# Performance work log

Hardware: AMD Instinct MI355X
Metric: run time of the kernel (lower is better)

Reference implementation:

```python
import jax, jax.numpy as jnp
import numpy as np


def setup_inputs() -> dict:
    key = jax.random.key(0)
    b, l, d_model, n_head, topk = 2, 2048, 1024, 16, 32
    dh = d_model // n_head
    k0, k1, k2, k3, k4 = jax.random.split(key, 5)
    s = 1.0 / np.sqrt(d_model)
    return {
        "q_in": jax.random.normal(k0, (b, l, d_model), jnp.float32),
        "kv_in": jax.random.normal(k1, (b, l, d_model), jnp.float32),
        "w_q": jax.random.normal(k2, (d_model, d_model), jnp.float32) * s,
        "w_kv": jax.random.normal(k3, (d_model, 2 * dh), jnp.float32) * s,
        "w_concat": jax.random.normal(k4, (d_model, d_model), jnp.float32) * s,
        "topk": topk,
        "n_head": n_head,
    }


def _l2norm_seq(x):
    # F.normalize default dim=1 -> normalize along the sequence axis (faithful to source)
    n = jnp.sqrt(jnp.sum(x * x, axis=1, keepdims=True))
    return x / jnp.maximum(n, 1e-12)


def reference(q_in, kv_in, w_q, w_kv, w_concat, topk, n_head):
    b, l, d_model = q_in.shape
    dh = d_model // n_head
    scale = 1.0 / np.sqrt(dh)

    q = q_in @ w_q                                  # (b, l, d_model)
    kv = kv_in @ w_kv                               # (b, l, 2*dh)
    k, v = kv[..., :dh], kv[..., dh:]
    k, v = _l2norm_seq(k), _l2norm_seq(v)           # (b, l, dh) single shared KV head

    q = q.reshape(b, l, n_head, dh).transpose(0, 2, 1, 3)  # (b, h, l, dh)

    # one similarity matrix reused for local attention and kNN retrieval
    sims = jnp.einsum('bhld,bmd->bhlm', q, k)       # (b, h, l, m)

    # local SDPA (KV head broadcast over query heads)
    local = jnp.einsum('bhlm,bmd->bhld', jax.nn.softmax(sims * scale, axis=-1), v)

    # exact inner-product kNN over stored keys (faiss memory stores k only,
    # so retrieved key == retrieved value == nearest stored key vectors)
    _, idx = jax.lax.top_k(sims, topk)              # (b, h, l, topk)
    mem = jax.vmap(lambda kk, ii: kk[ii])(k, idx)   # (b, h, l, topk, dh)

    s_ret = jnp.einsum('bhld,bhltd->bhlt', q, mem) * scale
    retrieved = jnp.einsum('bhlt,bhltd->bhld', jax.nn.softmax(s_ret, axis=-1), mem)

    out = (local + retrieved).transpose(0, 2, 1, 3).reshape(b, l, d_model)
    return out @ w_concat
```

## Files before the change

kernel.cpp:

```cpp
#include <hip/hip_runtime.h>
#include <cstddef>
#include <cstring>

#define B_    2
#define L_    2048
#define DM_   1024
#define NH_   16
#define DH_   64
#define SCALE_ 0.125f

typedef __bf16 bf16x8 __attribute__((ext_vector_type(8)));
typedef float  f32x4  __attribute__((ext_vector_type(4)));
typedef unsigned short ushort8v __attribute__((ext_vector_type(8)));
typedef unsigned short ushort4v __attribute__((ext_vector_type(4)));
typedef unsigned long long u64;
typedef unsigned int u32;

__device__ __forceinline__ u32 flipf(float f) {
    u32 u = __float_as_uint(f);
    return (u & 0x80000000u) ? ~u : (u | 0x80000000u);
}
__device__ __forceinline__ float bf2f(unsigned short u) {
    return __uint_as_float(((u32)u) << 16);
}
__device__ __forceinline__ unsigned short f2bf(float f) {
    __bf16 h = (__bf16)f;
    unsigned short u;
    __builtin_memcpy(&u, &h, 2);
    return u;
}
__device__ __forceinline__ u32 flip16(unsigned short u) {
    return (u & 0x8000u) ? (u32)(~u & 0xffffu) : (u32)(u | 0x8000u);
}
__device__ __forceinline__ unsigned short unflip16(u32 k) {
    return (k & 0x8000u) ? (unsigned short)(k ^ 0x8000u) : (unsigned short)(~k & 0xffffu);
}

__global__ __launch_bounds__(256)
void wsplit3(const float* __restrict__ W, unsigned short* __restrict__ w1,
             unsigned short* __restrict__ w2, unsigned short* __restrict__ w3,
             int K, int N) {
    const int n0 = blockIdx.x << 6;
    const int k0 = blockIdx.y << 6;
    const int t  = threadIdx.x;
    __shared__ float s[64][65];
    const int rr = t >> 4;
    const int c4 = (t & 15) << 2;
    #pragma unroll
    for (int rep = 0; rep < 4; ++rep) {
        int k = rr + (rep << 4);
        float4 x = *(const float4*)(W + (size_t)(k0 + k) * N + n0 + c4);
        s[k][c4+0] = x.x; s[k][c4+1] = x.y; s[k][c4+2] = x.z; s[k][c4+3] = x.w;
    }
    __syncthreads();
    #pragma unroll
    for (int rep = 0; rep < 4; ++rep) {
        int n = rr + (rep << 4);
        ushort4v h, m, l;
        #pragma unroll
        for (int j = 0; j < 4; ++j) {
            float x = s[c4 + j][n];
            unsigned short hh = f2bf(x);
            float r = x - bf2f(hh);
            unsigned short mm = f2bf(r);
            float r2 = r - bf2f(mm);
            h[j] = hh; m[j] = mm; l[j] = f2bf(r2);
        }
        size_t o = (size_t)(n0 + n) * K + k0 + c4;
        *(ushort4v*)(w1 + o) = h;
        *(ushort4v*)(w2 + o) = m;
        *(ushort4v*)(w3 + o) = l;
    }
}

__global__ __launch_bounds__(256)
void gemm6p(const float* __restrict__ A, const unsigned short* __restrict__ w1,
            const unsigned short* __restrict__ w2, const unsigned short* __restrict__ w3,
            float* __restrict__ C, int N, int K) {
    __shared__ __align__(16) unsigned short sA[3][128][40];
    __shared__ __align__(16) unsigned short sW[3][64][40];
    const int t    = threadIdx.x;
    const int wv   = t >> 6;
    const int lane = t & 63;
    const int quad = lane >> 4;
    const int n15  = lane & 15;
    const int bm = blockIdx.y << 7;
    const int bn = blockIdx.x << 6;
    const int wm = (wv >> 1) << 6;
    const int wn = (wv & 1) << 5;
    f32x4 acc[4][2];
    #pragma unroll
    for (int i = 0; i < 4; ++i)
        #pragma unroll
        for (int j = 0; j < 2; ++j)
            #pragma unroll
            for (int r = 0; r < 4; ++r) acc[i][j][r] = 0.f;

    const int ar  = t >> 1,  acg = (t & 1) << 4;
    const int wr  = t >> 2,  wcg = (t & 3) << 3;
    const float* Ap = A + (size_t)(bm + ar) * K + acg;
    const size_t wo = (size_t)(bn + wr) * K + wcg;

    for (int k0 = 0; k0 < K; k0 += 32) {
        float4 a0 = *(const float4*)(Ap + k0);
        float4 a1 = *(const float4*)(Ap + k0 + 4);
        float4 a2 = *(const float4*)(Ap + k0 + 8);
        float4 a3 = *(const float4*)(Ap + k0 + 12);
        ushort8v u1 = *(const ushort8v*)(w1 + wo + k0);
        ushort8v u2 = *(const ushort8v*)(w2 + wo + k0);
        ushort8v u3 = *(const ushort8v*)(w3 + wo + k0);
        __syncthreads();
        {
            float av[16] = {a0.x,a0.y,a0.z,a0.w, a1.x,a1.y,a1.z,a1.w,
                            a2.x,a2.y,a2.z,a2.w, a3.x,a3.y,a3.z,a3.w};
            ushort8v h0, h1, m0, m1, lo0, lo1;
            #pragma unroll
            for (int i = 0; i < 8; ++i) {
                float x = av[i];
                unsigned short hh = f2bf(x);
                float r = x - bf2f(hh);
                unsigned short mm = f2bf(r);
                h0[i] = hh; m0[i] = mm; lo0[i] = f2bf(r - bf2f(mm));
                float y = av[8 + i];
                unsigned short hh2 = f2bf(y);
                float r2 = y - bf2f(hh2);
                unsigned short mm2 = f2bf(r2);
                h1[i] = hh2; m1[i] = mm2; lo1[i] = f2bf(r2 - bf2f(mm2));
            }
            *(ushort8v*)&sA[0][ar][acg]     = h0;
            *(ushort8v*)&sA[0][ar][acg + 8] = h1;
            *(ushort8v*)&sA[1][ar][acg]     = m0;
            *(ushort8v*)&sA[1][ar][acg + 8] = m1;
            *(ushort8v*)&sA[2][ar][acg]     = lo0;
            *(ushort8v*)&sA[2][ar][acg + 8] = lo1;
            *(ushort8v*)&sW[0][wr][wcg] = u1;
            *(ushort8v*)&sW[1][wr][wcg] = u2;
            *(ushort8v*)&sW[2][wr][wcg] = u3;
        }
        __syncthreads();
        bf16x8 af[3][4];
        #pragma unroll
        for (int mi = 0; mi < 4; ++mi) {
            af[0][mi] = *(const bf16x8*)&sA[0][wm + (mi << 4) + n15][quad << 3];
            af[1][mi] = *(const bf16x8*)&sA[1][wm + (mi << 4) + n15][quad << 3];
            af[2][mi] = *(const bf16x8*)&sA[2][wm + (mi << 4) + n15][quad << 3];
        }
        #pragma unroll
        for (int nj = 0; nj < 2; ++nj) {
            bf16x8 wf1 = *(const bf16x8*)&sW[0][wn + (nj << 4) + n15][quad << 3];
            bf16x8 wf2 = *(const bf16x8*)&sW[1][wn + (nj << 4) + n15][quad << 3];
            bf16x8 wf3 = *(const bf16x8*)&sW[2][wn + (nj << 4) + n15][quad << 3];
            #pragma unroll
            for (int mi = 0; mi < 4; ++mi) {
                acc[mi][nj] = __builtin_amdgcn_mfma_f32_16x16x32_bf16(af[0][mi], wf1, acc[mi][nj], 0, 0, 0);
                acc[mi][nj] = __builtin_amdgcn_mfma_f32_16x16x32_bf16(af[0][mi], wf2, acc[mi][nj], 0, 0, 0);
                acc[mi][nj] = __builtin_amdgcn_mfma_f32_16x16x32_bf16(af[1][mi], wf1, acc[mi][nj], 0, 0, 0);
                acc[mi][nj] = __builtin_amdgcn_mfma_f32_16x16x32_bf16(af[1][mi], wf2, acc[mi][nj], 0, 0, 0);
                acc[mi][nj] = __builtin_amdgcn_mfma_f32_16x16x32_bf16(af[0][mi], wf3, acc[mi][nj], 0, 0, 0);
                acc[mi][nj] = __builtin_amdgcn_mfma_f32_16x16x32_bf16(af[2][mi], wf1, acc[mi][nj], 0, 0, 0);
            }
        }
    }
    #pragma unroll
    for (int mi = 0; mi < 4; ++mi)
        #pragma unroll
        for (int nj = 0; nj < 2; ++nj)
            #pragma unroll
            for (int r = 0; r < 4; ++r)
                C[(size_t)(bm + wm + (mi << 4) + (quad << 2) + r) * N
                  + bn + wn + (nj << 4) + n15] = acc[mi][nj][r];
}

__global__ __launch_bounds__(256)
void gemm3p(const float* __restrict__ A, const unsigned short* __restrict__ w1,
            const unsigned short* __restrict__ w2,
            float* __restrict__ C, int N, int K) {
    __shared__ __align__(16) unsigned short sA[2][128][40];
    __shared__ __align__(16) unsigned short sW[2][64][40];
    const int t    = threadIdx.x;
    const int wv   = t >> 6;
    const int lane = t & 63;
    const int quad = lane >> 4;
    const int n15  = lane & 15;
    const int bm = blockIdx.y << 7;
    const int bn = blockIdx.x << 6;
    const int wm = (wv >> 1) << 6;
    const int wn = (wv & 1) << 5;
    f32x4 acc[4][2];
    #pragma unroll
    for (int i = 0; i < 4; ++i)
        #pragma unroll
        for (int j = 0; j < 2; ++j)
            #pragma unroll
            for (int r = 0; r < 4; ++r) acc[i][j][r] = 0.f;

    const int ar  = t >> 1,  acg = (t & 1) << 4;
    const int wr  = t >> 2,  wcg = (t & 3) << 3;
    const float* Ap = A + (size_t)(bm + ar) * K + acg;
    const size_t wo = (size_t)(bn + wr) * K + wcg;

    for (int k0 = 0; k0 < K; k0 += 32) {
        float4 a0 = *(const float4*)(Ap + k0);
        float4 a1 = *(const float4*)(Ap + k0 + 4);
        float4 a2 = *(const float4*)(Ap + k0 + 8);
        float4 a3 = *(const float4*)(Ap + k0 + 12);
        ushort8v u1 = *(const ushort8v*)(w1 + wo + k0);
        ushort8v u2 = *(const ushort8v*)(w2 + wo + k0);
        __syncthreads();
        {
            float av[16] = {a0.x,a0.y,a0.z,a0.w, a1.x,a1.y,a1.z,a1.w,
                            a2.x,a2.y,a2.z,a2.w, a3.x,a3.y,a3.z,a3.w};
            ushort8v h0, h1, l0v, l1v;
            #pragma unroll
            for (int i = 0; i < 8; ++i) {
                float x = av[i];
                unsigned short hh = f2bf(x);
                h0[i] = hh; l0v[i] = f2bf(x - bf2f(hh));
                float y = av[8 + i];
                unsigned short hh2 = f2bf(y);
                h1[i] = hh2; l1v[i] = f2bf(y - bf2f(hh2));
            }
            *(ushort8v*)&sA[0][ar][acg]     = h0;
            *(ushort8v*)&sA[0][ar][acg + 8] = h1;
            *(ushort8v*)&sA[1][ar][acg]     = l0v;
            *(ushort8v*)&sA[1][ar][acg + 8] = l1v;
            *(ushort8v*)&sW[0][wr][wcg] = u1;
            *(ushort8v*)&sW[1][wr][wcg] = u2;
        }
        __syncthreads();
        bf16x8 af[2][4];
        #pragma unroll
        for (int mi = 0; mi < 4; ++mi) {
            af[0][mi] = *(const bf16x8*)&sA[0][wm + (mi << 4) + n15][quad << 3];
            af[1][mi] = *(const bf16x8*)&sA[1][wm + (mi << 4) + n15][quad << 3];
        }
        #pragma unroll
        for (int nj = 0; nj < 2; ++nj) {
            bf16x8 wf1 = *(const bf16x8*)&sW[0][wn + (nj << 4) + n15][quad << 3];
            bf16x8 wf2 = *(const bf16x8*)&sW[1][wn + (nj << 4) + n15][quad << 3];
            #pragma unroll
            for (int mi = 0; mi < 4; ++mi) {
                acc[mi][nj] = __builtin_amdgcn_mfma_f32_16x16x32_bf16(af[0][mi], wf1, acc[mi][nj], 0, 0, 0);
                acc[mi][nj] = __builtin_amdgcn_mfma_f32_16x16x32_bf16(af[0][mi], wf2, acc[mi][nj], 0, 0, 0);
                acc[mi][nj] = __builtin_amdgcn_mfma_f32_16x16x32_bf16(af[1][mi], wf1, acc[mi][nj], 0, 0, 0);
            }
        }
    }
    #pragma unroll
    for (int mi = 0; mi < 4; ++mi)
        #pragma unroll
        for (int nj = 0; nj < 2; ++nj)
            #pragma unroll
            for (int r = 0; r < 4; ++r)
                C[(size_t)(bm + wm + (mi << 4) + (quad << 2) + r) * N
                  + bn + wn + (nj << 4) + n15] = acc[mi][nj][r];
}

__global__ __launch_bounds__(256)
void col_norms(const float* __restrict__ kv, float* __restrict__ invn) {
    const int bc = blockIdx.x;
    const int b  = bc >> 7;
    const int c  = bc & 127;
    const int t  = threadIdx.x;
    const float* base = kv + (size_t)b * L_ * 128 + c;
    float ss = 0.f;
    for (int l = t; l < L_; l += 256) {
        float x = base[(size_t)l * 128];
        ss += x * x;
    }
    #pragma unroll
    for (int off = 32; off; off >>= 1) ss += __shfl_xor(ss, off);
    __shared__ float red[4];
    if ((t & 63) == 0) red[t >> 6] = ss;
    __syncthreads();
    if (t == 0) {
        float tot = red[0] + red[1] + red[2] + red[3];
        invn[bc] = 1.f / fmaxf(sqrtf(tot), 1e-12f);
    }
}

__global__ __launch_bounds__(256)
void scale_kv(const float* __restrict__ kv, const float* __restrict__ invn,
              float* __restrict__ kn, __bf16* __restrict__ kh,
              __bf16* __restrict__ vT) {
    const int b  = blockIdx.y;
    const int l0 = blockIdx.x << 6;
    const int t  = threadIdx.x;
    __shared__ float s_inv[128];
    __shared__ float s_vt[64][65];
    if (t < 128) s_inv[t] = invn[b * 128 + t];
    __syncthreads();
    #pragma unroll
    for (int rep = 0; rep < 8; ++rep) {
        int idx = (rep << 8) + t;
        int li  = idx >> 5;
        int c4  = (idx & 31) << 2;
        float4 x = *(const float4*)(kv + ((size_t)(b * L_ + l0 + li)) * 128 + c4);
        x.x *= s_inv[c4]; x.y *= s_inv[c4+1]; x.z *= s_inv[c4+2]; x.w *= s_inv[c4+3];
        if (c4 < 64) {
            size_t o = ((size_t)(b * L_ + l0 + li)) * DH_ + c4;
            *(float4*)(kn + o) = x;
            kh[o+0] = (__bf16)x.x; kh[o+1] = (__bf16)x.y;
            kh[o+2] = (__bf16)x.z; kh[o+3] = (__bf16)x.w;
        } else {
            int d = c4 - 64;
            s_vt[d+0][li] = x.x; s_vt[d+1][li] = x.y; s_vt[d+2][li] = x.z; s_vt[d+3][li] = x.w;
        }
    }
    __syncthreads();
    #pragma unroll
    for (int rep = 0; rep < 4; ++rep) {
        int idx = (rep << 8) + t;
        int d   = idx >> 4;
        int j   = (idx & 15) << 2;
        size_t o = ((size_t)b * DH_ + d) * L_ + l0 + j;
        vT[o+0] = (__bf16)s_vt[d][j+0];
        vT[o+1] = (__bf16)s_vt[d][j+1];
        vT[o+2] = (__bf16)s_vt[d][j+2];
        vT[o+3] = (__bf16)s_vt[d][j+3];
    }
}

#define SST2_ 1032

__global__ __launch_bounds__(256, 4)
void attn_part(const float* __restrict__ q,
               const __bf16* __restrict__ kh,
               const __bf16* __restrict__ vT,
               float* __restrict__ attn,
               u32* __restrict__ cand,
               int* __restrict__ candC) {
    const int tile = blockIdx.x;
    const int h    = blockIdx.y;
    const int b    = blockIdx.z;
    const int l0   = tile << 4;
    const int t    = threadIdx.x;
    const int w    = t >> 6;
    const int lane = t & 63;
    const int quad = lane >> 4;
    const int n15  = lane & 15;

    __shared__ unsigned short s_sims[16 * SST2_];
    __shared__ float s_local[16][66];
    __shared__ float s_denom[16];

    {
        float* sl = &s_local[0][0];
        for (int i = t; i < 16 * 66; i += 256) sl[i] = 0.f;
        if (t < 16) s_denom[t] = 0.f;
    }

    bf16x8 qf[2];
    {
        const float* qp = q + ((size_t)(b * L_ + l0 + n15)) * DM_ + h * DH_ + (quad << 3);
        #pragma unroll
        for (int ks = 0; ks < 2; ++ks) {
            float4 x0 = *(const float4*)(qp + (ks << 5));
            float4 x1 = *(const float4*)(qp + (ks << 5) + 4);
            float xv[8] = {x0.x, x0.y, x0.z, x0.w, x1.x, x1.y, x1.z, x1.w};
            #pragma unroll
            for (int i2 = 0; i2 < 8; ++i2) qf[ks][i2] = (__bf16)xv[i2];
        }
    }

    f32x4 accL[4] = {{0,0,0,0},{0,0,0,0},{0,0,0,0},{0,0,0,0}};
    float psum = 0.f;
    float bvmax[4] = {-3e38f, -3e38f, -3e38f, -3e38f};
    int   c0[4]    = {0, 0, 0, 0};
    const __bf16* khb = kh + (size_t)b * L_ * DH_;
    const __bf16* vtb = vT + (size_t)b * DH_ * L_;
    const int rg0 = ((b * NH_ + h) * L_) + l0;

    #pragma unroll 1
    for (int hf = 0; hf < 2; ++hf) {
        #pragma unroll
        for (int g = 0; g < 4; ++g) {
            bf16x8 kf[8];
            const __bf16* kp = khb + (size_t)((hf << 10) + (w << 8) + (g << 6) + n15) * DH_ + (quad << 3);
            #pragma unroll
            for (int jj = 0; jj < 4; ++jj) {
                kf[2*jj]   = *(const bf16x8*)(kp + (size_t)(jj << 4) * DH_);
                kf[2*jj+1] = *(const bf16x8*)(kp + (size_t)(jj << 4) * DH_ + 32);
            }
            #pragma unroll
            for (int jj = 0; jj < 4; ++jj) {
                int m0 = (w << 8) + (g << 6) + (jj << 4);
                f32x4 acc = {0.f, 0.f, 0.f, 0.f};
                acc = __builtin_amdgcn_mfma_f32_16x16x32_bf16(kf[2*jj],   qf[0], acc, 0, 0, 0);
                acc = __builtin_amdgcn_mfma_f32_16x16x32_bf16(kf[2*jj+1], qf[1], acc, 0, 0, 0);
                u32 lo = (u32)f2bf(acc[0]) | ((u32)f2bf(acc[1]) << 16);
                u32 hi = (u32)f2bf(acc[2]) | ((u32)f2bf(acc[3]) << 16);
                u64 pk = ((u64)hi << 32) | lo;
                *(u64*)(s_sims + (size_t)n15 * SST2_ + m0 + (quad << 2)) = pk;
            }
        }
        __syncthreads();

        #pragma unroll 1
        for (int rr2 = 0; rr2 < 4; ++rr2) {
            const int r = (w << 2) + rr2;
            const unsigned short* srow = s_sims + r * SST2_;
            ushort8v rv[2];
            rv[0] = *(const ushort8v*)(srow + (lane << 3));
            rv[1] = *(const ushort8v*)(srow + 512 + (lane << 3));
            float bv = -3e38f;
            #pragma unroll
            for (int j = 0; j < 2; ++j)
                #pragma unroll
                for (int e = 0; e < 8; ++e) bv = fmaxf(bv, bf2f(rv[j][e]));
            bvmax[rr2] = fmaxf(bvmax[rr2], bv);
            u32* cr = cand + (size_t)(rg0 + r) * 96;
            if (hf == 0) {
                u32 key = flip16(f2bf(bv));
                u32 thr = 0;
                #pragma unroll
                for (int bp = 15; bp >= 0; --bp) {
                    u32 tt = thr | (1u << bp);
                    if (__popcll(__ballot(key >= tt)) >= 32) thr = tt;
                }
                float thrv = bf2f(unflip16(thr)) - 0.01f;
                int base = 0;
                #pragma unroll
                for (int j = 0; j < 2; ++j) {
                    #pragma unroll
                    for (int e = 0; e < 8; ++e) {
                        bool pred = bf2f(rv[j][e]) >= thrv;
                        u64 mk = __ballot(pred);
                        if (pred) {
                            int pos = base + __popcll(mk & ((1ull << lane) - 1));
                            if (pos < 96)
                                cr[pos] = ((u32)rv[j][e] << 16)
                                        | (u32)((j << 9) + (lane << 3) + e);
                        }
                        base += __popcll(mk);
                    }
                }
                c0[rr2] = base < 96 ? base : 96;
            } else {
                u32 key = flip16(f2bf(bvmax[rr2]));
                u32 thr = 0;
                #pragma unroll
                for (int bp = 15; bp >= 0; --bp) {
                    u32 tt = thr | (1u << bp);
                    if (__popcll(__ballot(key >= tt)) >= 32) thr = tt;
                }
                float thrv = bf2f(unflip16(thr)) - 0.01f;
                const int cc0 = c0[rr2];
                u32 e0 = (lane < cc0) ? cr[lane] : 0u;
                u32 e1 = (64 + lane < cc0) ? cr[64 + lane] : 0u;
                int base = 0;
                {
                    bool pred = (lane < cc0)
                              && (bf2f((unsigned short)(e0 >> 16)) >= thrv);
                    u64 mk = __ballot(pred);
                    if (pred) {
                        int pos = __popcll(mk & ((1ull << lane) - 1));
                        cr[pos] = e0;
                    }
                    base = __popcll(mk);
                }
                if (cc0 > 64) {
                    bool pred = (64 + lane < cc0)
                              && (bf2f((unsigned short)(e1 >> 16)) >= thrv);
                    u64 mk = __ballot(pred);
                    if (pred) {
                        int pos = base + __popcll(mk & ((1ull << lane) - 1));
                        if (pos < 96) cr[pos] = e1;
                    }
                    base += __popcll(mk);
                }
                #pragma unroll
                for (int j = 0; j < 2; ++j) {
                    #pragma unroll
                    for (int e = 0; e < 8; ++e) {
                        bool pred = bf2f(rv[j][e]) >= thrv;
                        u64 mk = __ballot(pred);
                        if (pred) {
                            int pos = base + __popcll(mk & ((1ull << lane) - 1));
                            if (pos < 96)
                                cr[pos] = ((u32)rv[j][e] << 16)
                                        | (u32)(1024 + (j << 9) + (lane << 3) + e);
                        }
                        base += __popcll(mk);
                    }
                }
                if (lane == 0) candC[rg0 + r] = base < 96 ? base : 96;
            }
        }

        #pragma unroll
        for (int g = 0; g < 4; ++g) {
            bf16x8 bvv[2][4];
            #pragma unroll
            for (int t2 = 0; t2 < 2; ++t2)
                #pragma unroll
                for (int nn = 0; nn < 4; ++nn)
                    bvv[t2][nn] = *(const bf16x8*)(vtb + (size_t)((nn << 4) + n15) * L_
                                  + (hf << 10) + (w << 8) + (g << 6) + (t2 << 5) + (quad << 3));
            #pragma unroll
            for (int t2 = 0; t2 < 2; ++t2) {
                int mb = (w << 8) + (g << 6) + (t2 << 5);
                ushort8v pu = *(const ushort8v*)(s_sims + n15 * SST2_ + mb + (quad << 3));
                bf16x8 af;
                #pragma unroll
                for (int e = 0; e < 8; ++e) {
                    float p = __expf(SCALE_ * bf2f(pu[e]));
                    psum += p;
                    af[e] = (__bf16)p;
                }
                #pragma unroll
                for (int nn = 0; nn < 4; ++nn)
                    accL[nn] = __builtin_amdgcn_mfma_f32_16x16x32_bf16(af, bvv[t2][nn], accL[nn], 0, 0, 0);
            }
        }
        __syncthreads();
    }

    psum += __shfl_xor(psum, 16);
    psum += __shfl_xor(psum, 32);
    if (lane < 16) atomicAdd(&s_denom[lane], psum);
    #pragma unroll
    for (int nn = 0; nn < 4; ++nn)
        #pragma unroll
        for (int rr = 0; rr < 4; ++rr)
            atomicAdd(&s_local[(quad << 2) + rr][(nn << 4) + n15], accL[nn][rr]);
    __syncthreads();

    {
        int r  = t >> 4;
        int d0 = (t & 15) << 2;
        float inv = 1.f / s_denom[r];
        float* op = attn + ((size_t)(b * L_ + l0 + r)) * DM_ + h * DH_ + d0;
        op[0] = s_local[r][d0+0] * inv;
        op[1] = s_local[r][d0+1] * inv;
        op[2] = s_local[r][d0+2] * inv;
        op[3] = s_local[r][d0+3] * inv;
    }
}

__global__ __launch_bounds__(256)
void topk_merge(const float* __restrict__ q, const float* __restrict__ kn,
                const u32* __restrict__ cand, const int* __restrict__ candC,
                float* __restrict__ attn) {
    const int wv   = threadIdx.x >> 6;
    const int lane = threadIdx.x & 63;
    const int row  = (blockIdx.x << 2) + wv;
    const int l = row & (L_ - 1);
    const int h = (row >> 11) & (NH_ - 1);
    const int b = row >> 15;
    __shared__ float s_dot[4][96];
    __shared__ __align__(16) u64 s_sel[4][32];

    const int C = candC[row];
    const u32* cr = cand + (size_t)row * 96;
    const float* knb = kn + (size_t)b * L_ * DH_;
    const float* qr  = q + ((size_t)(b * L_ + l)) * DM_ + h * DH_;

    int mreg0 = (lane < C) ? (int)(cr[lane] & 0xffffu) : 0;
    int mreg1 = (64 + lane < C) ? (int)(cr[64 + lane] & 0xffffu) : 0;

    const int cg = lane >> 4;
    const int dg = lane & 15;
    float4 qx = *(const float4*)(qr + (dg << 2));

    #pragma unroll 2
    for (int base = 0; base < C; base += 4) {
        int ci = base + cg;
        int src = ci & 63;
        int mA = __shfl(mreg0, src);
        int mB = __shfl(mreg1, src);
        int m  = (ci < 64) ? mA : mB;
        float4 kx = *(const float4*)(knb + (size_t)m * DH_ + (dg << 2));
        float p = kx.x * qx.x + kx.y * qx.y + kx.z * qx.z + kx.w * qx.w;
        p += __shfl_xor(p, 1);
        p += __shfl_xor(p, 2);
        p += __shfl_xor(p, 4);
        p += __shfl_xor(p, 8);
        if (dg == 0 && ci < C) s_dot[wv][ci] = p;
    }

    float dotA = (lane < C) ? s_dot[wv][lane] : 0.f;
    float dotB = (64 + lane < C) ? s_dot[wv][64 + lane] : 0.f;
    u32 keyA = (lane < C) ? flipf(dotA) : 0u;
    u32 keyB = (64 + lane < C) ? flipf(dotB) : 0u;

    u32 thr2 = 0;
    if (C <= 64) {
        #pragma unroll
        for (int bp = 31; bp >= 0; --bp) {
            u32 tt = thr2 | (1u << bp);
            if (__popcll(__ballot(keyA >= tt)) >= 32) thr2 = tt;
        }
    } else {
        #pragma unroll
        for (int bp = 31; bp >= 0; --bp) {
            u32 tt = thr2 | (1u << bp);
            int c2 = __popcll(__ballot(keyA >= tt)) + __popcll(__ballot(keyB >= tt));
            if (c2 >= 32) thr2 = tt;
        }
    }
    {
        bool pA = keyA >= thr2;
        u64 mkA = __ballot(pA);
        if (pA) {
            int pos = __popcll(mkA & ((1ull << lane) - 1));
            if (pos < 32) {
                float pt = __expf(SCALE_ * dotA);
                s_sel[wv][pos] = ((u64)__float_as_uint(pt) << 32) | (u32)mreg0;
            }
        }
        if (C > 64) {
            int cA = __popcll(mkA);
            bool pB = keyB >= thr2;
            u64 mkB = __ballot(pB);
            if (pB) {
                int pos = cA + __popcll(mkB & ((1ull << lane) - 1));
                if (pos < 32) {
                    float pt = __expf(SCALE_ * dotB);
                    s_sel[wv][pos] = ((u64)__float_as_uint(pt) << 32) | (u32)mreg1;
                }
            }
        }
    }
    {
        float pts[32];
        int   ms[32];
        #pragma unroll
        for (int i = 0; i < 32; ++i) {
            u64 s0 = s_sel[wv][i];
            pts[i] = __uint_as_float((u32)(s0 >> 32));
            ms[i]  = (int)(u32)(s0 & 0xffffffffu);
        }
        const float* knb2 = knb + lane;
        float kvv[32];
        #pragma unroll
        for (int i = 0; i < 32; ++i) kvv[i] = knb2[(size_t)ms[i] * DH_];
        float rs = 0.f, ret = 0.f;
        #pragma unroll
        for (int i = 0; i < 16; ++i) {
            rs  += pts[2*i] + pts[2*i+1];
            ret += pts[2*i] * kvv[2*i] + pts[2*i+1] * kvv[2*i+1];
        }
        size_t oa = ((size_t)(b * L_ + l)) * DM_ + h * DH_ + lane;
        attn[oa] = attn[oa] + ret / rs;
    }
}

extern "C" void kernel_launch(void* const* d_in, const int* in_sizes, int n_in,
                              void* d_out, int out_size, void* d_ws, size_t ws_size,
                              hipStream_t stream) {
    const float* q_in     = (const float*)d_in[0];
    const float* kv_in    = (const float*)d_in[1];
    const float* w_q      = (const float*)d_in[2];
    const float* w_kv     = (const float*)d_in[3];
    const float* w_concat = (const float*)d_in[4];
    float* out = (float*)d_out;

    float* ws   = (float*)d_ws;
    float* q    = ws;
    float* attn = ws + 4194304;
    float* kv   = attn;
    float* kn   = ws + 8388608;
    float* invn = ws + 8650752;
    unsigned short* us = (unsigned short*)(ws + 8651008);
    unsigned short* kh_u = us;
    unsigned short* vT_u = us + 262144;
    unsigned short* wq1  = us + 524288;
    unsigned short* wq2  = wq1 + 1048576;
    unsigned short* wq3  = wq2 + 1048576;
    unsigned short* wc1  = wq3 + 1048576;
    unsigned short* wc2  = wc1 + 1048576;
    unsigned short* wkv1 = wc2 + 1048576;
    unsigned short* wkv2 = wkv1 + 131072;
    unsigned short* wkv3 = wkv2 + 131072;
    u32* cand = (u32*)(wkv3 + 131072);
    unsigned short* wc3 = (unsigned short*)cand;
    int* candC = (int*)(cand + 65536 * 96);
    __bf16* kh = (__bf16*)kh_u;
    __bf16* vT = (__bf16*)vT_u;

    wsplit3<<<dim3(DM_ / 64, DM_ / 64), 256, 0, stream>>>(w_q, wq1, wq2, wq3, DM_, DM_);
    wsplit3<<<dim3(DM_ / 64, DM_ / 64), 256, 0, stream>>>(w_concat, wc1, wc2, wc3, DM_, DM_);
    wsplit3<<<dim3(128 / 64, DM_ / 64), 256, 0, stream>>>(w_kv, wkv1, wkv2, wkv3, DM_, 128);

    gemm6p<<<dim3(DM_ / 64, (B_ * L_) / 128), 256, 0, stream>>>(q_in, wq1, wq2, wq3, q, DM_, DM_);
    gemm6p<<<dim3(128 / 64, (B_ * L_) / 128), 256, 0, stream>>>(kv_in, wkv1, wkv2, wkv3, kv, 128, DM_);

    col_norms<<<B_ * 128, 256, 0, stream>>>(kv, invn);
    scale_kv<<<dim3(L_ / 64, B_), 256, 0, stream>>>(kv, invn, kn, kh, vT);

    attn_part<<<dim3(L_ / 16, NH_, B_), 256, 0, stream>>>(q, kh, vT, attn, cand, candC);
    topk_merge<<<(B_ * NH_ * L_) / 4, 256, 0, stream>>>(q, kn, cand, candC, attn);

    gemm3p<<<dim3(DM_ / 64, (B_ * L_) / 128), 256, 0, stream>>>(attn, wc1, wc2, out, DM_, DM_);
}
```

Before: 692.6 us.

## Swizzle sims LDS, alias finalize buffers, batch threshold search across rows

Replaces the padded sims shared buffer with an unpadded XOR-swizzled layout and aliases the finalize accumulators onto the same shared memory through a union. This cuts LDS use per block, and launch bounds are raised to 5 blocks per CU to use the freed space. The per-row max and the 16-step ballot threshold search are now interleaved across the four rows, and candidate loads are hoisted ahead of them to expose more instruction-level parallelism. Candidate indices are un-swizzled via lane^(r&7), which adds index arithmetic and register pressure under the tighter occupancy bound.

```diff
diff --git a/kernel.cpp b/kernel.cpp
--- a/kernel.cpp
+++ b/kernel.cpp
@@ -321,9 +321,7 @@
     }
 }
 
-#define SST2_ 1032
-
-__global__ __launch_bounds__(256, 4)
+__global__ __launch_bounds__(256, 5)
 void attn_part(const float* __restrict__ q,
                const __bf16* __restrict__ kh,
                const __bf16* __restrict__ vT,
@@ -340,15 +338,12 @@
     const int quad = lane >> 4;
     const int n15  = lane & 15;
 
-    __shared__ unsigned short s_sims[16 * SST2_];
-    __shared__ float s_local[16][66];
-    __shared__ float s_denom[16];
-
-    {
-        float* sl = &s_local[0][0];
-        for (int i = t; i < 16 * 66; i += 256) sl[i] = 0.f;
-        if (t < 16) s_denom[t] = 0.f;
-    }
+    __shared__ __align__(16) union SMem {
+        unsigned short sims[16 * 1024];
+        struct { float local[16][66]; float denom[16]; } fin;
+    } sm;
+    unsigned short* s_sims = sm.sims;
+    const int swz = n15 & 7;
 
     bf16x8 qf[2];
     {
@@ -391,95 +386,116 @@
                 u32 lo = (u32)f2bf(acc[0]) | ((u32)f2bf(acc[1]) << 16);
                 u32 hi = (u32)f2bf(acc[2]) | ((u32)f2bf(acc[3]) << 16);
                 u64 pk = ((u64)hi << 32) | lo;
-                *(u64*)(s_sims + (size_t)n15 * SST2_ + m0 + (quad << 2)) = pk;
+                int lb = (m0 << 1) + (quad << 3);
+                int pb = ((lb & ~15) ^ (swz << 4)) | (lb & 15);
+                *(u64*)((char*)s_sims + (n15 << 11) + pb) = pk;
             }
         }
         __syncthreads();
+
+        float bv[4];
+        #pragma unroll
+        for (int rr2 = 0; rr2 < 4; ++rr2) {
+            const unsigned short* srow = s_sims + (((w << 2) + rr2) << 10);
+            ushort8v a0 = *(const ushort8v*)(srow + (lane << 3));
+            ushort8v a1 = *(const ushort8v*)(srow + 512 + (lane << 3));
+            float b2 = -3e38f;
+            #pragma unroll
+            for (int e = 0; e < 8; ++e)
+                b2 = fmaxf(b2, fmaxf(bf2f(a0[e]), bf2f(a1[e])));
+            bv[rr2] = b2;
+            bvmax[rr2] = fmaxf(bvmax[rr2], b2);
+        }
+
+        u32 pe0[4], pe1[4];
+        if (hf) {
+            #pragma unroll
+            for (int rr2 = 0; rr2 < 4; ++rr2) {
+                const u32* cr = cand + (size_t)(rg0 + (w << 2) + rr2) * 96;
+                pe0[rr2] = (lane < c0[rr2]) ? cr[lane] : 0u;
+                pe1[rr2] = (64 + lane < c0[rr2]) ? cr[64 + lane] : 0u;
+            }
+        }
+
+        u32 thr[4] = {0, 0, 0, 0};
+        {
+            u32 key[4];
+            #pragma unroll
+            for (int rr2 = 0; rr2 < 4; ++rr2)
+                key[rr2] = flip16(f2bf(hf ? bvmax[rr2] : bv[rr2]));
+            #pragma unroll
+            for (int bp = 15; bp >= 0; --bp) {
+                #pragma unroll
+                for (int rr2 = 0; rr2 < 4; ++rr2) {
+                    u32 tt = thr[rr2] | (1u << bp);
+                    if (__popcll(__ballot(key[rr2] >= tt)) >= 32) thr[rr2] = tt;
+                }
+            }
+        }
 
         #pragma unroll 1
         for (int rr2 = 0; rr2 < 4; ++rr2) {
             const int r = (w << 2) + rr2;
-            const unsigned short* srow = s_sims + r * SST2_;
-            ushort8v rv[2];
-            rv[0] = *(const ushort8v*)(srow + (lane << 3));
-            rv[1] = *(const ushort8v*)(srow + 512 + (lane << 3));
-            float bv = -3e38f;
-            #pragma unroll
-            for (int j = 0; j < 2; ++j)
-                #pragma unroll
-                for (int e = 0; e < 8; ++e) bv = fmaxf(bv, bf2f(rv[j][e]));
-            bvmax[rr2] = fmaxf(bvmax[rr2], bv);
+            const unsigned short* srow = s_sims + (r << 10);
+            ushort8v rv0 = *(const ushort8v*)(srow + (lane << 3));
+            ushort8v rv1 = *(const ushort8v*)(srow + 512 + (lane << 3));
+            const int lx = (lane ^ (r & 7)) << 3;
+            float thrv = bf2f(unflip16(thr[rr2])) - 0.01f;
             u32* cr = cand + (size_t)(rg0 + r) * 96;
             if (hf == 0) {
-                u32 key = flip16(f2bf(bv));
-                u32 thr = 0;
-                #pragma unroll
-                for (int bp = 15; bp >= 0; --bp) {
-                    u32 tt = thr | (1u << bp);
-                    if (__popcll(__ballot(key >= tt)) >= 32) thr = tt;
-                }
-                float thrv = bf2f(unflip16(thr)) - 0.01f;
                 int base = 0;
                 #pragma unroll
                 for (int j = 0; j < 2; ++j) {
+                    ushort8v rv = j ? rv1 : rv0;
                     #pragma unroll
                     for (int e = 0; e < 8; ++e) {
-                        bool pred = bf2f(rv[j][e]) >= thrv;
+                        bool pred = bf2f(rv[e]) >= thrv;
                         u64 mk = __ballot(pred);
                         if (pred) {
                             int pos = base + __popcll(mk & ((1ull << lane) - 1));
                             if (pos < 96)
-                                cr[pos] = ((u32)rv[j][e] << 16)
-                                        | (u32)((j << 9) + (lane << 3) + e);
+                                cr[pos] = ((u32)rv[e] << 16)
+                                        | (u32)((j << 9) + lx + e);
                         }
                         base += __popcll(mk);
                     }
                 }
                 c0[rr2] = base < 96 ? base : 96;
             } else {
-                u32 key = flip16(f2bf(bvmax[rr2]));
-                u32 thr = 0;
-                #pragma unroll
-                for (int bp = 15; bp >= 0; --bp) {
-                    u32 tt = thr | (1u << bp);
-                    if (__popcll(__ballot(key >= tt)) >= 32) thr = tt;
-                }
-                float thrv = bf2f(unflip16(thr)) - 0.01f;
                 const int cc0 = c0[rr2];
-                u32 e0 = (lane < cc0) ? cr[lane] : 0u;
-                u32 e1 = (64 + lane < cc0) ? cr[64 + lane] : 0u;
                 int base = 0;
                 {
                     bool pred = (lane < cc0)
-                              && (bf2f((unsigned short)(e0 >> 16)) >= thrv);
+                              && (bf2f((unsigned short)(pe0[rr2] >> 16)) >= thrv);
                     u64 mk = __ballot(pred);
                     if (pred) {
                         int pos = __popcll(mk & ((1ull << lane) - 1));
-                        cr[pos] = e0;
+                        cr[pos] = pe0[rr2];
                     }
                     base = __popcll(mk);
                 }
                 if (cc0 > 64) {
                     bool pred = (64 + lane < cc0)
-                              && (bf2f((unsigned short)(e1 >> 16)) >= thrv);
+                              && (bf2f((unsigned short)(pe1[rr2] >> 16)) >= thrv);
                     u64 mk = __ballot(pred);
                     if (pred) {
                         int pos = base + __popcll(mk & ((1ull << lane) - 1));
-                        if (pos < 96) cr[pos] = e1;
+                        if (pos < 96) cr[pos] = pe1[rr2];
                     }
                     base += __popcll(mk);
                 }
                 #pragma unroll
                 for (int j = 0; j < 2; ++j) {
+                    ushort8v rv = j ? rv1 : rv0;
                     #pragma unroll
                     for (int e = 0; e < 8; ++e) {
-                        bool pred = bf2f(rv[j][e]) >= thrv;
+                        bool pred = bf2f(rv[e]) >= thrv;
                         u64 mk = __ballot(pred);
                         if (pred) {
                             int pos = base + __popcll(mk & ((1ull << lane) - 1));
                             if (pos < 96)
-                                cr[pos] = ((u32)rv[j][e] << 16)
-                                        | (u32)(1024 + (j << 9) + (lane << 3) + e);
+                                cr[pos] = ((u32)rv[e] << 16)
+                                        | (u32)(1024 + (j << 9) + lx + e);
                         }
                         base += __popcll(mk);
                     }
@@ -500,7 +516,8 @@
             #pragma unroll
             for (int t2 = 0; t2 < 2; ++t2) {
                 int mb = (w << 8) + (g << 6) + (t2 << 5);
-                ushort8v pu = *(const ushort8v*)(s_sims + n15 * SST2_ + mb + (quad << 3));
+                int unit = (mb >> 3) + quad;
+                ushort8v pu = *(const ushort8v*)(s_sims + (n15 << 10) + ((unit ^ swz) << 3));
                 bf16x8 af;
                 #pragma unroll
                 for (int e = 0; e < 8; ++e) {
@@ -516,25 +533,32 @@
         __syncthreads();
     }
 
+    {
+        float* sl = &sm.fin.local[0][0];
+        #pragma unroll 1
+        for (int i = t; i < 16 * 66 + 16; i += 256) sl[i] = 0.f;
+    }
+    __syncthreads();
+
     psum += __shfl_xor(psum, 16);
     psum += __shfl_xor(psum, 32);
-    if (lane < 16) atomicAdd(&s_denom[lane], psum);
+    if (lane < 16) atomicAdd(&sm.fin.denom[lane], psum);
     #pragma unroll
     for (int nn = 0; nn < 4; ++nn)
         #pragma unroll
         for (int rr = 0; rr < 4; ++rr)
-            atomicAdd(&s_local[(quad << 2) + rr][(nn << 4) + n15], accL[nn][rr]);
+            atomicAdd(&sm.fin.local[(quad << 2) + rr][(nn << 4) + n15], accL[nn][rr]);
     __syncthreads();
 
     {
         int r  = t >> 4;
         int d0 = (t & 15) << 2;
-        float inv = 1.f / s_denom[r];
+        float inv = 1.f / sm.fin.denom[r];
         float* op = attn + ((size_t)(b * L_ + l0 + r)) * DM_ + h * DH_ + d0;
-        op[0] = s_local[r][d0+0] * inv;
-        op[1] = s_local[r][d0+1] * inv;
-        op[2] = s_local[r][d0+2] * inv;
-        op[3] = s_local[r][d0+3] * inv;
+        op[0] = sm.fin.local[r][d0+0] * inv;
+        op[1] = sm.fin.local[r][d0+1] * inv;
+        op[2] = sm.fin.local[r][d0+2] * inv;
+        op[3] = sm.fin.local[r][d0+3] * inv;
     }
 }
 
```

Measured after the change: 751.0 us. 8.4% more time.

## Pre-split activations into bf16 planes and swizzle attention LDS scores

Applied to the files above, without the earlier changes.

Adds standalone asplit3/asplit2 kernels that split fp32 activations into bf16 hi/mid/lo planes once, so the GEMMs stop redoing that split in every column block. In exchange the GEMMs read three bf16 planes instead of one fp32 tile, and each split pass adds an extra write and read of the activations. attn_part now overlays the score tile and the reduction scratch in a shared-memory union, XOR-swizzles the score layout to cut bank conflicts, and keeps the provisional top-k candidates in LDS rather than global memory. The split planes reuse the candidate workspace region once it is free.

```diff
diff --git a/kernel.cpp b/kernel.cpp
--- a/kernel.cpp
+++ b/kernel.cpp
@@ -74,8 +74,49 @@
 }
 
 __global__ __launch_bounds__(256)
-void gemm6p(const float* __restrict__ A, const unsigned short* __restrict__ w1,
-            const unsigned short* __restrict__ w2, const unsigned short* __restrict__ w3,
+void asplit3(const float* __restrict__ X, unsigned short* __restrict__ p1,
+             unsigned short* __restrict__ p2, unsigned short* __restrict__ p3) {
+    const size_t i = ((size_t)blockIdx.x * 256 + threadIdx.x) * 8;
+    float4 x0 = *(const float4*)(X + i);
+    float4 x1 = *(const float4*)(X + i + 4);
+    float xv[8] = {x0.x, x0.y, x0.z, x0.w, x1.x, x1.y, x1.z, x1.w};
+    ushort8v h, m, l;
+    #pragma unroll
+    for (int e = 0; e < 8; ++e) {
+        float x = xv[e];
+        unsigned short hh = f2bf(x);
+        float r = x - bf2f(hh);
+        unsigned short mm = f2bf(r);
+        h[e] = hh; m[e] = mm; l[e] = f2bf(r - bf2f(mm));
+    }
+    *(ushort8v*)(p1 + i) = h;
+    *(ushort8v*)(p2 + i) = m;
+    *(ushort8v*)(p3 + i) = l;
+}
+
+__global__ __launch_bounds__(256)
+void asplit2(const float* __restrict__ X, unsigned short* __restrict__ p1,
+             unsigned short* __restrict__ p2) {
+    const size_t i = ((size_t)blockIdx.x * 256 + threadIdx.x) * 8;
+    float4 x0 = *(const float4*)(X + i);
+    float4 x1 = *(const float4*)(X + i + 4);
+    float xv[8] = {x0.x, x0.y, x0.z, x0.w, x1.x, x1.y, x1.z, x1.w};
+    ushort8v h, l;
+    #pragma unroll
+    for (int e = 0; e < 8; ++e) {
+        float x = xv[e];
+        unsigned short hh = f2bf(x);
+        h[e] = hh; l[e] = f2bf(x - bf2f(hh));
+    }
+    *(ushort8v*)(p1 + i) = h;
+    *(ushort8v*)(p2 + i) = l;
+}
+
+__global__ __launch_bounds__(256)
+void gemm6p(const unsigned short* __restrict__ a1, const unsigned short* __restrict__ a2,
+            const unsigned short* __restrict__ a3,
+            const unsigned short* __restrict__ w1, const unsigned short* __restrict__ w2,
+            const unsigned short* __restrict__ w3,
             float* __restrict__ C, int N, int K) {
     __shared__ __align__(16) unsigned short sA[3][128][40];
     __shared__ __align__(16) unsigned short sW[3][64][40];
@@ -98,45 +139,29 @@
 
     const int ar  = t >> 1,  acg = (t & 1) << 4;
     const int wr  = t >> 2,  wcg = (t & 3) << 3;
-    const float* Ap = A + (size_t)(bm + ar) * K + acg;
+    const size_t ao = (size_t)(bm + ar) * K + acg;
     const size_t wo = (size_t)(bn + wr) * K + wcg;
 
     for (int k0 = 0; k0 < K; k0 += 32) {
-        float4 a0 = *(const float4*)(Ap + k0);
-        float4 a1 = *(const float4*)(Ap + k0 + 4);
-        float4 a2 = *(const float4*)(Ap + k0 + 8);
-        float4 a3 = *(const float4*)(Ap + k0 + 12);
+        ushort8v A1a = *(const ushort8v*)(a1 + ao + k0);
+        ushort8v A1b = *(const ushort8v*)(a1 + ao + k0 + 8);
+        ushort8v A2a = *(const ushort8v*)(a2 + ao + k0);
+        ushort8v A2b = *(const ushort8v*)(a2 + ao + k0 + 8);
+        ushort8v A3a = *(const ushort8v*)(a3 + ao + k0);
+        ushort8v A3b = *(const ushort8v*)(a3 + ao + k0 + 8);
         ushort8v u1 = *(const ushort8v*)(w1 + wo + k0);
         ushort8v u2 = *(const ushort8v*)(w2 + wo + k0);
         ushort8v u3 = *(const ushort8v*)(w3 + wo + k0);
         __syncthreads();
-        {
-            float av[16] = {a0.x,a0.y,a0.z,a0.w, a1.x,a1.y,a1.z,a1.w,
-                            a2.x,a2.y,a2.z,a2.w, a3.x,a3.y,a3.z,a3.w};
-            ushort8v h0, h1, m0, m1, lo0, lo1;
-            #pragma unroll
-            for (int i = 0; i < 8; ++i) {
-                float x = av[i];
-                unsigned short hh = f2bf(x);
-                float r = x - bf2f(hh);
-                unsigned short mm = f2bf(r);
-                h0[i] = hh; m0[i] = mm; lo0[i] = f2bf(r - bf2f(mm));
-                float y = av[8 + i];
-                unsigned short hh2 = f2bf(y);
-                float r2 = y - bf2f(hh2);
-                unsigned short mm2 = f2bf(r2);
-                h1[i] = hh2; m1[i] = mm2; lo1[i] = f2bf(r2 - bf2f(mm2));
-            }
-            *(ushort8v*)&sA[0][ar][acg]     = h0;
-            *(ushort8v*)&sA[0][ar][acg + 8] = h1;
-            *(ushort8v*)&sA[1][ar][acg]     = m0;
-            *(ushort8v*)&sA[1][ar][acg + 8] = m1;
-            *(ushort8v*)&sA[2][ar][acg]     = lo0;
-            *(ushort8v*)&sA[2][ar][acg + 8] = lo1;
-            *(ushort8v*)&sW[0][wr][wcg] = u1;
-            *(ushort8v*)&sW[1][wr][wcg] = u2;
-            *(ushort8v*)&sW[2][wr][wcg] = u3;
-        }
+        *(ushort8v*)&sA[0][ar][acg]     = A1a;
+        *(ushort8v*)&sA[0][ar][acg + 8] = A1b;
+        *(ushort8v*)&sA[1][ar][acg]     = A2a;
+        *(ushort8v*)&sA[1][ar][acg + 8] = A2b;
+        *(ushort8v*)&sA[2][ar][acg]     = A3a;
+        *(ushort8v*)&sA[2][ar][acg + 8] = A3b;
+        *(ushort8v*)&sW[0][wr][wcg] = u1;
+        *(ushort8v*)&sW[1][wr][wcg] = u2;
+        *(ushort8v*)&sW[2][wr][wcg] = u3;
         __syncthreads();
         bf16x8 af[3][4];
         #pragma unroll
@@ -172,8 +197,8 @@
 }
 
 __global__ __launch_bounds__(256)
-void gemm3p(const float* __restrict__ A, const unsigned short* __restrict__ w1,
-            const unsigned short* __restrict__ w2,
+void gemm3p(const unsigned short* __restrict__ a1, const unsigned short* __restrict__ a2,
+            const unsigned short* __restrict__ w1, const unsigned short* __restrict__ w2,
             float* __restrict__ C, int N, int K) {
     __shared__ __align__(16) unsigned short sA[2][128][40];
     __shared__ __align__(16) unsigned short sW[2][64][40];
@@ -196,37 +221,23 @@
 
     const int ar  = t >> 1,  acg = (t & 1) << 4;
     const int wr  = t >> 2,  wcg = (t & 3) << 3;
-    const float* Ap = A + (size_t)(bm + ar) * K + acg;
+    const size_t ao = (size_t)(bm + ar) * K + acg;
     const size_t wo = (size_t)(bn + wr) * K + wcg;
 
     for (int k0 = 0; k0 < K; k0 += 32) {
-        float4 a0 = *(const float4*)(Ap + k0);
-        float4 a1 = *(const float4*)(Ap + k0 + 4);
-        float4 a2 = *(const float4*)(Ap + k0 + 8);
-        float4 a3 = *(const float4*)(Ap + k0 + 12);
+        ushort8v A1a = *(const ushort8v*)(a1 + ao + k0);
+        ushort8v A1b = *(const ushort8v*)(a1 + ao + k0 + 8);
+        ushort8v A2a = *(const ushort8v*)(a2 + ao + k0);
+        ushort8v A2b = *(const ushort8v*)(a2 + ao + k0 + 8);
         ushort8v u1 = *(const ushort8v*)(w1 + wo + k0);
         ushort8v u2 = *(const ushort8v*)(w2 + wo + k0);
         __syncthreads();
-        {
-            float av[16] = {a0.x,a0.y,a0.z,a0.w, a1.x,a1.y,a1.z,a1.w,
-                            a2.x,a2.y,a2.z,a2.w, a3.x,a3.y,a3.z,a3.w};
-            ushort8v h0, h1, l0v, l1v;
-            #pragma unroll
-            for (int i = 0; i < 8; ++i) {
-                float x = av[i];
-                unsigned short hh = f2bf(x);
-                h0[i] = hh; l0v[i] = f2bf(x - bf2f(hh));
-                float y = av[8 + i];
-                unsigned short hh2 = f2bf(y);
-                h1[i] = hh2; l1v[i] = f2bf(y - bf2f(hh2));
-            }
-            *(ushort8v*)&sA[0][ar][acg]     = h0;
-            *(ushort8v*)&sA[0][ar][acg + 8] = h1;
-            *(ushort8v*)&sA[1][ar][acg]     = l0v;
-            *(ushort8v*)&sA[1][ar][acg + 8] = l1v;
-            *(ushort8v*)&sW[0][wr][wcg] = u1;
-            *(ushort8v*)&sW[1][wr][wcg] = u2;
-        }
+        *(ushort8v*)&sA[0][ar][acg]     = A1a;
+        *(ushort8v*)&sA[0][ar][acg + 8] = A1b;
+        *(ushort8v*)&sA[1][ar][acg]     = A2a;
+        *(ushort8v*)&sA[1][ar][acg + 8] = A2b;
+        *(ushort8v*)&sW[0][wr][wcg] = u1;
+        *(ushort8v*)&sW[1][wr][wcg] = u2;
         __syncthreads();
         bf16x8 af[2][4];
         #pragma unroll
@@ -320,8 +331,6 @@
         vT[o+3] = (__bf16)s_vt[d][j+3];
     }
 }
-
-#define SST2_ 1032
 
 __global__ __launch_bounds__(256, 4)
 void attn_part(const float* __restrict__ q,
@@ -340,15 +349,13 @@
     const int quad = lane >> 4;
     const int n15  = lane & 15;
 
-    __shared__ unsigned short s_sims[16 * SST2_];
-    __shared__ float s_local[16][66];
-    __shared__ float s_denom[16];
-
-    {
-        float* sl = &s_local[0][0];
-        for (int i = t; i < 16 * 66; i += 256) sl[i] = 0.f;
-        if (t < 16) s_denom[t] = 0.f;
-    }
+    __shared__ __align__(16) union SMem {
+        unsigned short sims[16 * 1024];
+        struct { float local[16][66]; float denom[16]; } fin;
+    } sm;
+    __shared__ u32 s_prov[16][96];
+    unsigned short* s_sims = sm.sims;
+    const int swz = n15 & 7;
 
     bf16x8 qf[2];
     {
@@ -391,7 +398,9 @@
                 u32 lo = (u32)f2bf(acc[0]) | ((u32)f2bf(acc[1]) << 16);
                 u32 hi = (u32)f2bf(acc[2]) | ((u32)f2bf(acc[3]) << 16);
                 u64 pk = ((u64)hi << 32) | lo;
-                *(u64*)(s_sims + (size_t)n15 * SST2_ + m0 + (quad << 2)) = pk;
+                int lb = (m0 << 1) + (quad << 3);
+                int pb = ((lb & ~15) ^ (swz << 4)) | (lb & 15);
+                *(u64*)((char*)s_sims + (n15 << 11) + pb) = pk;
             }
         }
         __syncthreads();
@@ -399,17 +408,17 @@
         #pragma unroll 1
         for (int rr2 = 0; rr2 < 4; ++rr2) {
             const int r = (w << 2) + rr2;
-            const unsigned short* srow = s_sims + r * SST2_;
+            const unsigned short* srow = s_sims + (r << 10);
             ushort8v rv[2];
             rv[0] = *(const ushort8v*)(srow + (lane << 3));
             rv[1] = *(const ushort8v*)(srow + 512 + (lane << 3));
+            const int lx = (lane ^ (r & 7)) << 3;
             float bv = -3e38f;
             #pragma unroll
             for (int j = 0; j < 2; ++j)
                 #pragma unroll
                 for (int e = 0; e < 8; ++e) bv = fmaxf(bv, bf2f(rv[j][e]));
             bvmax[rr2] = fmaxf(bvmax[rr2], bv);
-            u32* cr = cand + (size_t)(rg0 + r) * 96;
             if (hf == 0) {
                 u32 key = flip16(f2bf(bv));
                 u32 thr = 0;
@@ -429,8 +438,8 @@
                         if (pred) {
                             int pos = base + __popcll(mk & ((1ull << lane) - 1));
                             if (pos < 96)
-                                cr[pos] = ((u32)rv[j][e] << 16)
-                                        | (u32)((j << 9) + (lane << 3) + e);
+                                s_prov[r][pos] = ((u32)rv[j][e] << 16)
+                                               | (u32)((j << 9) + lx + e);
                         }
                         base += __popcll(mk);
                     }
@@ -446,8 +455,9 @@
                 }
                 float thrv = bf2f(unflip16(thr)) - 0.01f;
                 const int cc0 = c0[rr2];
-                u32 e0 = (lane < cc0) ? cr[lane] : 0u;
-                u32 e1 = (64 + lane < cc0) ? cr[64 + lane] : 0u;
+                u32 e0 = (lane < cc0) ? s_prov[r][lane] : 0u;
+                u32 e1 = (64 + lane < cc0) ? s_prov[r][64 + lane] : 0u;
+                u32* cr = cand + (size_t)(rg0 + r) * 96;
                 int base = 0;
                 {
                     bool pred = (lane < cc0)
@@ -479,7 +489,7 @@
                             int pos = base + __popcll(mk & ((1ull << lane) - 1));
                             if (pos < 96)
                                 cr[pos] = ((u32)rv[j][e] << 16)
-                                        | (u32)(1024 + (j << 9) + (lane << 3) + e);
+                                        | (u32)(1024 + (j << 9) + lx + e);
                         }
                         base += __popcll(mk);
                     }
@@ -500,7 +510,8 @@
             #pragma unroll
             for (int t2 = 0; t2 < 2; ++t2) {
                 int mb = (w << 8) + (g << 6) + (t2 << 5);
-                ushort8v pu = *(const ushort8v*)(s_sims + n15 * SST2_ + mb + (quad << 3));
+                int unit = (mb >> 3) + quad;
+                ushort8v pu = *(const ushort8v*)(s_sims + (n15 << 10) + ((unit ^ swz) << 3));
                 bf16x8 af;
                 #pragma unroll
                 for (int e = 0; e < 8; ++e) {
@@ -516,25 +527,32 @@
         __syncthreads();
     }
 
+    {
+        float* sl = &sm.fin.local[0][0];
+        #pragma unroll 1
+        for (int i = t; i < 16 * 66 + 16; i += 256) sl[i] = 0.f;
+    }
+    __syncthreads();
+
     psum += __shfl_xor(psum, 16);
     psum += __shfl_xor(psum, 32);
-    if (lane < 16) atomicAdd(&s_denom[lane], psum);
+    if (lane < 16) atomicAdd(&sm.fin.denom[lane], psum);
     #pragma unroll
     for (int nn = 0; nn < 4; ++nn)
         #pragma unroll
         for (int rr = 0; rr < 4; ++rr)
-            atomicAdd(&s_local[(quad << 2) + rr][(nn << 4) + n15], accL[nn][rr]);
+            atomicAdd(&sm.fin.local[(quad << 2) + rr][(nn << 4) + n15], accL[nn][rr]);
     __syncthreads();
 
     {
         int r  = t >> 4;
         int d0 = (t & 15) << 2;
-        float inv = 1.f / s_denom[r];
+        float inv = 1.f / sm.fin.denom[r];
         float* op = attn + ((size_t)(b * L_ + l0 + r)) * DM_ + h * DH_ + d0;
-        op[0] = s_local[r][d0+0] * inv;
-        op[1] = s_local[r][d0+1] * inv;
-        op[2] = s_local[r][d0+2] * inv;
-        op[3] = s_local[r][d0+3] * inv;
+        op[0] = sm.fin.local[r][d0+0] * inv;
+        op[1] = sm.fin.local[r][d0+1] * inv;
+        op[2] = sm.fin.local[r][d0+2] * inv;
+        op[3] = sm.fin.local[r][d0+3] * inv;
     }
 }
 
@@ -674,17 +692,25 @@
     unsigned short* wkv2 = wkv1 + 131072;
     unsigned short* wkv3 = wkv2 + 131072;
     u32* cand = (u32*)(wkv3 + 131072);
-    unsigned short* wc3 = (unsigned short*)cand;
     int* candC = (int*)(cand + 65536 * 96);
     __bf16* kh = (__bf16*)kh_u;
     __bf16* vT = (__bf16*)vT_u;
 
+    unsigned short* r1 = (unsigned short*)cand;
+    unsigned short* ap1 = r1;
+    unsigned short* ap2 = r1 + 4194304;
+    unsigned short* ap3 = r1 + 8388608;
+    unsigned short* wc3 = ap1;
+
     wsplit3<<<dim3(DM_ / 64, DM_ / 64), 256, 0, stream>>>(w_q, wq1, wq2, wq3, DM_, DM_);
     wsplit3<<<dim3(DM_ / 64, DM_ / 64), 256, 0, stream>>>(w_concat, wc1, wc2, wc3, DM_, DM_);
     wsplit3<<<dim3(128 / 64, DM_ / 64), 256, 0, stream>>>(w_kv, wkv1, wkv2, wkv3, DM_, 128);
 
-    gemm6p<<<dim3(DM_ / 64, (B_ * L_) / 128), 256, 0, stream>>>(q_in, wq1, wq2, wq3, q, DM_, DM_);
-    gemm6p<<<dim3(128 / 64, (B_ * L_) / 128), 256, 0, stream>>>(kv_in, wkv1, wkv2, wkv3, kv, 128, DM_);
+    asplit3<<<(B_ * L_ * DM_) / 2048, 256, 0, stream>>>(q_in, ap1, ap2, ap3);
+    gemm6p<<<dim3(DM_ / 64, (B_ * L_) / 128), 256, 0, stream>>>(ap1, ap2, ap3, wq1, wq2, wq3, q, DM_, DM_);
+
+    asplit3<<<(B_ * L_ * DM_) / 2048, 256, 0, stream>>>(kv_in, ap1, ap2, ap3);
+    gemm6p<<<dim3(128 / 64, (B_ * L_) / 128), 256, 0, stream>>>(ap1, ap2, ap3, wkv1, wkv2, wkv3, kv, 128, DM_);
 
     col_norms<<<B_ * 128, 256, 0, stream>>>(kv, invn);
     scale_kv<<<dim3(L_ / 64, B_), 256, 0, stream>>>(kv, invn, kn, kh, vT);
@@ -692,5 +718,6 @@
     attn_part<<<dim3(L_ / 16, NH_, B_), 256, 0, stream>>>(q, kh, vT, attn, cand, candC);
     topk_merge<<<(B_ * NH_ * L_) / 4, 256, 0, stream>>>(q, kn, cand, candC, attn);
 
-    gemm3p<<<dim3(DM_ / 64, (B_ * L_) / 128), 256, 0, stream>>>(attn, wc1, wc2, out, DM_, DM_);
-}
+    asplit2<<<(B_ * L_ * DM_) / 2048, 256, 0, stream>>>(attn, ap1, ap2);
+    gemm3p<<<dim3(DM_ / 64, (B_ * L_) / 128), 256, 0, stream>>>(ap1, ap2, wc1, wc2, out, DM_, DM_);
+}
```

After: 709.5 us. 2.4% more time.
